# Performance work log

Measured on AMD Instinct MI355X. Metric: run time of the kernel, lower is better.

The kernel has to match this reference:

```python
import math
import jax, jax.numpy as jnp
import numpy as np

B, D, T, C, H = 4096, 1024, 768, 16, 4
CURV = 0.05
EPS = 1e-8
ASINH_MAX = float(np.arcsinh(2.0 ** 15))

# ---------- Poincare ball ops (hyptorch.pmath) ----------

def artanh(x):
    x = jnp.clip(x, -1 + 1e-5, 1 - 1e-5)
    return 0.5 * (jnp.log1p(x) - jnp.log1p(-x))

def p_logmap0(y, c):
    sc = c ** 0.5
    n = jnp.clip(jnp.linalg.norm(y, axis=-1, keepdims=True), 1e-15, None)
    return y / (n * sc) * artanh(sc * n)

def p_expmap0(u, c):
    sc = c ** 0.5
    n = jnp.clip(jnp.linalg.norm(u, axis=-1, keepdims=True), 1e-15, None)
    return jnp.tanh(sc * n) * u / (sc * n)

def p_project(x, c):
    maxn = (1 - 4e-3) / c ** 0.5  # float32 eps in hyptorch
    n = jnp.clip(jnp.linalg.norm(x, axis=-1, keepdims=True), 1e-15, None)
    return jnp.where(n > maxn, x / n * maxn, x)

# ---------- Lorentz ops (MERU-style L module) ----------

def l_expmap0(x, c):
    rc = (c ** 0.5) * jnp.linalg.norm(x, axis=-1, keepdims=True)
    si = jnp.clip(rc, EPS, ASINH_MAX)
    return jnp.sinh(si) * x / jnp.clip(rc, EPS, None)

def l_logmap0(x, c):
    rc = (c ** 0.5) * jnp.linalg.norm(x, axis=-1, keepdims=True)
    return jnp.arcsinh(rc) * x / jnp.clip(rc, EPS, None)

def oxy_angle(x, y, c):
    xt = jnp.sqrt(1.0 / c + jnp.sum(x * x, -1))
    yt = jnp.sqrt(1.0 / c + jnp.sum(y * y, -1))
    c_xyl = c * (jnp.sum(x * y, -1) - xt * yt)
    num = yt + c_xyl * xt
    den = jnp.sqrt(jnp.clip(c_xyl ** 2 - 1.0, EPS, None))
    acos_in = num / (jnp.linalg.norm(x, axis=-1) * den + EPS)
    return jnp.arccos(jnp.clip(acos_in, -1 + EPS, 1 - EPS))

def half_aperture(x, c, min_radius=0.1):
    asin_in = 2.0 * min_radius / (jnp.linalg.norm(x, axis=-1) * c ** 0.5 + EPS)
    return jnp.arcsin(jnp.clip(asin_in, -1 + EPS, 1 - EPS))

# ---------- small building blocks ----------

def layernorm(x, w, b, eps=1e-5):
    mu = jnp.mean(x, -1, keepdims=True)
    var = jnp.mean((x - mu) ** 2, -1, keepdims=True)
    return (x - mu) * jax.lax.rsqrt(var + eps) * w + b

def mha(x, w_in, b_in, w_out, b_out):
    # x: (B, S=4, D), torch nn.MultiheadAttention, batch_first, 4 heads
    Bq, S, Dm = x.shape
    hd = Dm // H
    qkv = x @ w_in.T + b_in
    q, k, v = jnp.split(qkv, 3, axis=-1)
    rs = lambda t: t.reshape(Bq, S, H, hd).transpose(0, 2, 1, 3)
    q, k, v = rs(q), rs(k), rs(v)
    a = jax.nn.softmax(jnp.einsum('bhqd,bhkd->bhqk', q, k) / math.sqrt(hd), axis=-1)
    o = jnp.einsum('bhqk,bhkd->bhqd', a, v).transpose(0, 2, 1, 3).reshape(Bq, S, Dm)
    return o @ w_out.T + b_out

def mobius_add_batch(x, y, c):
    # x: (C, D) (the -p points), y: (B, D) -> (C, B, D)
    xy = x @ y.T                               # (C, B)
    x2 = jnp.sum(x * x, -1, keepdims=True)     # (C, 1)
    y2 = jnp.sum(y * y, -1)                    # (B,)
    num = (1 + 2 * c * xy + c * y2[None, :])[..., None] * x[:, None, :] \
        + (1 - c * x2)[..., None] * y[None, :, :]
    den = 1 + 2 * c * xy + c * c * x2 * y2[None, :]
    return num / (den[..., None] + 1e-5)

def hyperbolic_mlr(x, a, p, c):
    sc = c ** 0.5
    p_p = p_expmap0(p, c)                      # (C, D)
    conf = 1 - c * jnp.sum(p_p ** 2, -1, keepdims=True)
    a_p = a * conf                             # (C, D)
    lam = 2.0 / (1 - c * jnp.sum(p_p ** 2, -1))
    a_norm = jnp.linalg.norm(a_p, axis=-1)     # (C,)
    kk = lam * a_norm / sc
    mob = mobius_add_batch(-p_p, x, c)         # (C, B, D)
    num = 2 * sc * jnp.einsum('cbd,cd->cb', mob, a_p)
    den = a_norm[:, None] * (1 - c * jnp.sum(mob ** 2, -1))
    return (kk[:, None] * jnp.arcsinh(num / den)).T  # (B, C)

def hyp_loss_fn(order_hyp, family_hyp, order, family, mask,
                to_w, to_b, tf_w, tf_b):
    order_feats = l_expmap0(order @ to_w.T + to_b, CURV)
    order_loss = jnp.mean(jax.nn.relu(
        oxy_angle(order_feats, family_hyp, CURV) - half_aperture(order_feats, CURV)))
    fam_feats = l_expmap0(family @ tf_w.T + tf_b, CURV)
    fpen = jax.nn.relu(
        oxy_angle(fam_feats, order_hyp, CURV) - half_aperture(fam_feats, CURV))
    m = mask.astype(order.dtype)
    cnt = jnp.sum(m)
    family_loss = jnp.where(cnt > 0, jnp.sum(fpen * m) / jnp.clip(cnt, 1.0, None), 0.0)
    return order_loss + family_loss


def setup_inputs() -> dict:
    key = jax.random.key(0)
    ks = jax.random.split(key, 20)
    g = lambda k, s, sc: jax.random.normal(k, s, jnp.float32) * sc
    inp = {
        # Poincare-ball points: scale down so sqrt(c)*||x|| << 1
        'order_hyp': g(ks[0], (B, D), 0.02),
        'family_hyp': g(ks[1], (B, D), 0.02),
        'order_euc': g(ks[2], (B, D), 1.0),
        'family_euc': g(ks[3], (B, D), 1.0),
        'order': g(ks[4], (B, T), 1.0),
        'family': g(ks[5], (B, T), 1.0),
        'mask': jax.random.randint(ks[6], (B,), 0, 2, jnp.int32),
        # MultiheadAttention params
        'in_proj_w': g(ks[7], (3 * D, D), D ** -0.5),
        'in_proj_b': jnp.zeros((3 * D,), jnp.float32),
        'out_proj_w': g(ks[8], (D, D), D ** -0.5),
        'out_proj_b': jnp.zeros((D,), jnp.float32),
        # LayerNorm
        'ln_w': jnp.ones((D,), jnp.float32),
        'ln_b': jnp.zeros((D,), jnp.float32),
        # text projections
        'to_w': g(ks[9], (D, T), T ** -0.5),
        'to_b': jnp.zeros((D,), jnp.float32),
        'tf_w': g(ks[10], (D, T), T ** -0.5),
        'tf_b': jnp.zeros((D,), jnp.float32),
        # HyperbolicMLR params
        'mlr_a': g(ks[11], (C, D), 0.02),
        'mlr_p': g(ks[12], (C, D), 0.02),
    }
    return inp


def reference(order_hyp, family_hyp, order_euc, family_euc, order, family, mask,
              in_proj_w, in_proj_b, out_proj_w, out_proj_b, ln_w, ln_b,
              to_w, to_b, tf_w, tf_b, mlr_a, mlr_p):
    # FromPoincare (logmap0 on the ball)
    fh_e = p_logmap0(family_hyp, CURV)
    oh_e = p_logmap0(order_hyp, CURV)
    gf = jnp.stack([oh_e, fh_e, order_euc, family_euc], axis=1)  # (B, 4, D)
    attn = mha(gf, in_proj_w, in_proj_b, out_proj_w, out_proj_b)
    gf = layernorm(gf + attn, ln_w, ln_b)
    oh, fh, oeu, feu = gf[:, 0], gf[:, 1], gf[:, 2], gf[:, 3]
    fh = l_expmap0(fh, CURV)
    oh = l_expmap0(oh, CURV)
    hyp_loss = hyp_loss_fn(oh, fh, order, family, mask, to_w, to_b, tf_w, tf_b)
    oh_out = l_logmap0(oh, CURV)
    hyp_pt = p_project(p_expmap0(oh_out, CURV), CURV)  # ToPoincare(riemannian=False)
    logits = hyperbolic_mlr(hyp_pt, mlr_a, mlr_p, CURV)
    return (logits, hyp_loss, oh, fh, oeu, feu)
```

## Files before the change

kernel.cpp:

```cpp
#include <hip/hip_runtime.h>
#include <stdint.h>

#define BB    4096
#define DD    1024
#define TT    768
#define CC    16
#define HH    4
#define SS    4
#define HD    256
#define M1    (BB*SS)
#define CURVF 0.05f
#define SCF   0.22360679774997896f
#define EPSF  1e-8f
#define ASINH_MAXF 11.090354888959125f

#define OFF_LOGITS 0ull
#define OFF_LOSS   65536ull
#define OFF_OH     65537ull
#define OFF_FH     (65537ull + 4194304ull)
#define OFF_OEU    (65537ull + 2ull*4194304ull)
#define OFF_FEU    (65537ull + 3ull*4194304ull)

typedef __attribute__((ext_vector_type(8))) short bf16x8;
typedef __attribute__((ext_vector_type(4))) float f32x4;

__device__ __forceinline__ float bf2f(unsigned short h) {
  union { unsigned int u; float f; } v; v.u = ((unsigned int)h) << 16; return v.f;
}
__device__ __forceinline__ unsigned short f2bf(float f) {
  union { float f; unsigned int u; } v; v.f = f;
  unsigned int u = v.u;
  return (unsigned short)((u + 0x7FFFu + ((u >> 16) & 1u)) >> 16);
}
__device__ __forceinline__ ushort4 f2bf4(float4 v) {
  ushort4 o; o.x = f2bf(v.x); o.y = f2bf(v.y); o.z = f2bf(v.z); o.w = f2bf(v.w);
  return o;
}
__device__ __forceinline__ float wsum(float v) {
#pragma unroll
  for (int o = 32; o > 0; o >>= 1) v += __shfl_xor(v, o, 64);
  return v;
}
__device__ __forceinline__ float block_sum(float v, float* red) {
  v = wsum(v);
  int lane = threadIdx.x & 63, wv = threadIdx.x >> 6;
  __syncthreads();
  if (lane == 0) red[wv] = v;
  __syncthreads();
  return red[0] + red[1] + red[2] + red[3];
}
__device__ __forceinline__ float artanh_clip(float x) {
  x = fminf(fmaxf(x, -1.0f + 1e-5f), 1.0f - 1e-5f);
  return 0.5f * (log1pf(x) - log1pf(-x));
}

typedef __attribute__((address_space(1))) const void gas_void;
typedef __attribute__((address_space(3))) void las_void;
__device__ __forceinline__ void gld16(void* l, const void* g) {
  __builtin_amdgcn_global_load_lds((gas_void*)g, (las_void*)l, 16, 0, 0);
}

#define VMCNT(n) asm volatile("s_waitcnt vmcnt(" #n ")" ::: "memory")

struct Cvt6 {
  const float4* src[6];
  unsigned short* dst[6];
  unsigned int end4[6];
};

__device__ __forceinline__ void prep_gf_body(const float* __restrict__ ohyp,
    const float* __restrict__ fhyp, const float* __restrict__ oeuc,
    const float* __restrict__ feuc, unsigned short* __restrict__ gf,
    int b, float* red) {
  int t = threadIdx.x;
  size_t base4 = (size_t)b * (DD / 4);
  float4 xo = ((const float4*)ohyp)[base4 + t];
  float4 xf = ((const float4*)fhyp)[base4 + t];
  float so = xo.x * xo.x + xo.y * xo.y + xo.z * xo.z + xo.w * xo.w;
  float sf = xf.x * xf.x + xf.y * xf.y + xf.z * xf.z + xf.w * xf.w;
  float no2 = block_sum(so, red);
  float nf2 = block_sum(sf, red);
  float no = fmaxf(sqrtf(no2), 1e-15f);
  float nf = fmaxf(sqrtf(nf2), 1e-15f);
  float fo = artanh_clip(SCF * no) / (no * SCF);
  float ff = artanh_clip(SCF * nf) / (nf * SCF);
  size_t g0 = (size_t)b * 4 * (DD / 4);
  float4 e2 = ((const float4*)oeuc)[base4 + t];
  float4 e3 = ((const float4*)feuc)[base4 + t];
  float4 y0 = {xo.x * fo, xo.y * fo, xo.z * fo, xo.w * fo};
  float4 y1 = {xf.x * ff, xf.y * ff, xf.z * ff, xf.w * ff};
  ((ushort4*)gf)[g0 + t]              = f2bf4(y0);
  ((ushort4*)gf)[g0 + DD / 4 + t]     = f2bf4(y1);
  ((ushort4*)gf)[g0 + 2 * DD / 4 + t] = f2bf4(e2);
  ((ushort4*)gf)[g0 + 3 * DD / 4 + t] = f2bf4(e3);
}

__device__ __forceinline__ void mlr_prep_body(const float* __restrict__ a,
    const float* __restrict__ p, float* __restrict__ p_p, float* __restrict__ a_p,
    float* __restrict__ cs, int c, float* red) {
  int t = threadIdx.x;
  size_t base4 = (size_t)c * (DD / 4);
  float4 pv = ((const float4*)p)[base4 + t];
  float4 av = ((const float4*)a)[base4 + t];
  float sp = pv.x * pv.x + pv.y * pv.y + pv.z * pv.z + pv.w * pv.w;
  float sa = av.x * av.x + av.y * av.y + av.z * av.z + av.w * av.w;
  float spa = pv.x * av.x + pv.y * av.y + pv.z * av.z + pv.w * av.w;
  sp = block_sum(sp, red); sa = block_sum(sa, red); spa = block_sum(spa, red);
  float n = fmaxf(sqrtf(sp), 1e-15f);
  float f = tanhf(SCF * n) / (SCF * n);
  float x2 = f * f * sp;
  float conf = 1.0f - CURVF * x2;
  float a_norm = fabsf(conf) * sqrtf(sa);
  float lam = 2.0f / (1.0f - CURVF * x2);
  float kk = lam * a_norm / SCF;
  float xa = -f * conf * spa;
  float4 pp = {pv.x * f, pv.y * f, pv.z * f, pv.w * f};
  float4 ap = {av.x * conf, av.y * conf, av.z * conf, av.w * conf};
  ((float4*)p_p)[base4 + t] = pp;
  ((float4*)a_p)[base4 + t] = ap;
  if (threadIdx.x == 0) {
    cs[c * 5 + 0] = x2; cs[c * 5 + 1] = conf; cs[c * 5 + 2] = a_norm;
    cs[c * 5 + 3] = kk; cs[c * 5 + 4] = xa;
  }
}

__global__ __launch_bounds__(256) void k_front(
    const float* __restrict__ ohyp, const float* __restrict__ fhyp,
    const float* __restrict__ oeuc, const float* __restrict__ feuc,
    unsigned short* __restrict__ gf,
    const float* __restrict__ mlr_a, const float* __restrict__ mlr_p,
    float* __restrict__ p_p, float* __restrict__ a_p, float* __restrict__ cs,
    Cvt6 cv, unsigned int total4) {
  __shared__ float red[4];
  unsigned int blk = blockIdx.x;
  if (blk < BB) {
    prep_gf_body(ohyp, fhyp, oeuc, feuc, gf, (int)blk, red);
    return;
  }
  if (blk < BB + CC) {
    mlr_prep_body(mlr_a, mlr_p, p_p, a_p, cs, (int)(blk - BB), red);
    return;
  }
  unsigned int i = (blk - BB - CC) * 256 + threadIdx.x;
  if (i >= total4) return;
#pragma unroll
  for (int j = 0; j < 6; j++) {
    if (i < cv.end4[j]) {
      unsigned int k = i - (j ? cv.end4[j - 1] : 0u);
      ((ushort4*)cv.dst[j])[k] = f2bf4(cv.src[j][k]);
      return;
    }
  }
}

__device__ __forceinline__ void gemm256_body(
    const unsigned short* __restrict__ A, const unsigned short* __restrict__ Bm,
    const float* __restrict__ bias, void* __restrict__ Cv,
    int N, int K, int bx, int by, int out_bf16,
    unsigned short (*lds)[2][8192]) {
  const long tileM = (long)by * 256;
  const long tileN = (long)bx * 256;
  const int tid = threadIdx.x;
  const int lane = tid & 63;
  const int wv = tid >> 6;
  const int wr = wv >> 2;
  const int wc = wv & 3;
  const int NT = K >> 5;

  f32x4 acc[8][4];
#pragma unroll
  for (int i = 0; i < 8; i++)
#pragma unroll
    for (int j = 0; j < 4; j++) acc[i][j] = (f32x4){0.f, 0.f, 0.f, 0.f};

  const int srow = tid >> 2;
  const int lc = (tid & 3) ^ ((srow >> 1) & 3);
  const unsigned short* Ag = A + (tileM + srow) * (long)K + lc * 8;
  const unsigned short* Bg = Bm + (tileN + srow) * (long)K + lc * 8;

  auto stageA = [&](int t) {
    int b = t & 3;
    const unsigned short* s = Ag + t * 32;
    gld16(&lds[b][0][tid * 8], s);
    gld16(&lds[b][0][4096 + tid * 8], s + (long)128 * K);
  };
  auto stageB = [&](int t) {
    int b = t & 3;
    const unsigned short* s = Bg + t * 32;
    gld16(&lds[b][1][tid * 8], s);
    gld16(&lds[b][1][4096 + tid * 8], s + (long)128 * K);
  };

  stageA(0); stageB(0);
  stageA(1); stageB(1);
  stageA(2); stageB(2);
  VMCNT(8);
  __builtin_amdgcn_s_barrier();
  asm volatile("" ::: "memory");

  const int fr = lane & 15;
  const int hi = lane >> 4;
  const int fko = (hi ^ ((fr >> 1) & 3)) * 8;

  for (int t = 0; t < NT; ++t) {
    const unsigned short* Ab = &lds[t & 3][0][0];
    const unsigned short* Bb = &lds[t & 3][1][0];
    bf16x8 af[4], bfr[4];
#pragma unroll
    for (int j = 0; j < 4; j++)
      bfr[j] = *(const bf16x8*)(Bb + (wc * 64 + j * 16 + fr) * 32 + fko);
#pragma unroll
    for (int i = 0; i < 4; i++)
      af[i] = *(const bf16x8*)(Ab + (wr * 128 + i * 16 + fr) * 32 + fko);
    if (t + 3 < NT) stageA(t + 3);
    __builtin_amdgcn_s_setprio(1);
#pragma unroll
    for (int i = 0; i < 4; i++)
#pragma unroll
      for (int j = 0; j < 4; j++)
        acc[i][j] = __builtin_amdgcn_mfma_f32_16x16x32_bf16(af[i], bfr[j], acc[i][j], 0, 0, 0);
    __builtin_amdgcn_s_setprio(0);
#pragma unroll
    for (int i = 0; i < 4; i++)
      af[i] = *(const bf16x8*)(Ab + (wr * 128 + (i + 4) * 16 + fr) * 32 + fko);
    if (t + 3 < NT) stageB(t + 3);
    __builtin_amdgcn_s_setprio(1);
#pragma unroll
    for (int i = 0; i < 4; i++)
#pragma unroll
      for (int j = 0; j < 4; j++)
        acc[i + 4][j] = __builtin_amdgcn_mfma_f32_16x16x32_bf16(af[i], bfr[j], acc[i + 4][j], 0, 0, 0);
    __builtin_amdgcn_s_setprio(0);
    if (t + 1 < NT) {
      if (t + 3 < NT)      VMCNT(8);
      else if (t + 2 < NT) VMCNT(4);
      else                 VMCNT(0);
      __builtin_amdgcn_s_barrier();
      asm volatile("" ::: "memory");
    }
  }

  const int er = hi * 4;
  if (out_bf16) {
#pragma unroll
    for (int i = 0; i < 8; i++)
#pragma unroll
      for (int j = 0; j < 4; j++) {
        long col = tileN + wc * 64 + j * 16 + fr;
        float bv = bias ? bias[col] : 0.f;
#pragma unroll
        for (int r = 0; r < 4; r++) {
          long row = tileM + wr * 128 + i * 16 + er + r;
          ((unsigned short*)Cv)[row * (long)N + col] = f2bf(acc[i][j][r] + bv);
        }
      }
  } else {
#pragma unroll
    for (int i = 0; i < 8; i++)
#pragma unroll
      for (int j = 0; j < 4; j++) {
        long col = tileN + wc * 64 + j * 16 + fr;
        float bv = bias ? bias[col] : 0.f;
#pragma unroll
        for (int r = 0; r < 4; r++) {
          long row = tileM + wr * 128 + i * 16 + er + r;
          ((float*)Cv)[row * (long)N + col] = acc[i][j][r] + bv;
        }
      }
  }
}

template <int OUT_BF16>
__global__ __launch_bounds__(512) void k_gemm256(
    const unsigned short* __restrict__ A, const unsigned short* __restrict__ Bm,
    const float* __restrict__ bias, void* __restrict__ Cv,
    int N, int K, int nx) {
  __shared__ unsigned short lds[4][2][8192];
  const int nwg = gridDim.x;
  const int rid = blockIdx.x;
  const int wg = (rid & 7) * (nwg >> 3) + (rid >> 3);
  gemm256_body(A, Bm, bias, Cv, N, K, wg % nx, wg / nx, OUT_BF16, lds);
}

__global__ __launch_bounds__(512) void k_gemm_merged(
    const unsigned short* __restrict__ A0, const unsigned short* __restrict__ B0,
    const float* __restrict__ bias0, void* __restrict__ C0, int N0, int K0,
    int nx0, int nwg0,
    const unsigned short* __restrict__ A1, const unsigned short* __restrict__ B1,
    const float* __restrict__ bias1, void* __restrict__ C1,
    const unsigned short* __restrict__ A2, const unsigned short* __restrict__ B2,
    const float* __restrict__ bias2, void* __restrict__ C2,
    int N12, int K12, int nx12, int nwg1) {
  __shared__ unsigned short lds[4][2][8192];
  const int nwg = gridDim.x;
  const int rid = blockIdx.x;
  const int wg = (rid & 7) * (nwg >> 3) + (rid >> 3);
  if (wg < nwg0) {
    gemm256_body(A0, B0, bias0, C0, N0, K0, wg % nx0, wg / nx0, 1, lds);
  } else if (wg < nwg0 + nwg1) {
    int w = wg - nwg0;
    gemm256_body(A1, B1, bias1, C1, N12, K12, w % nx12, w / nx12, 0, lds);
  } else {
    int w = wg - nwg0 - nwg1;
    gemm256_body(A2, B2, bias2, C2, N12, K12, w % nx12, w / nx12, 0, lds);
  }
}

__global__ __launch_bounds__(256) void k_attn(const unsigned short* __restrict__ qkv,
                                              unsigned short* __restrict__ o) {
  int b = blockIdx.x;
  int h = blockIdx.y;
  int lane = threadIdx.x & 63;
  int qi = threadIdx.x >> 6;
  const unsigned short* base = qkv + (size_t)b * 4 * 3072 + h * HD;
  int d = lane * 4;
  float qv[4], kv[4][4], vv[4][4];
  {
    ushort4 q4 = *(const ushort4*)(base + (size_t)qi * 3072 + d);
    qv[0] = bf2f(q4.x); qv[1] = bf2f(q4.y); qv[2] = bf2f(q4.z); qv[3] = bf2f(q4.w);
  }
#pragma unroll
  for (int j = 0; j < 4; j++) {
    ushort4 k4 = *(const ushort4*)(base + (size_t)j * 3072 + 1024 + d);
    ushort4 v4 = *(const ushort4*)(base + (size_t)j * 3072 + 2048 + d);
    kv[j][0] = bf2f(k4.x); kv[j][1] = bf2f(k4.y); kv[j][2] = bf2f(k4.z); kv[j][3] = bf2f(k4.w);
    vv[j][0] = bf2f(v4.x); vv[j][1] = bf2f(v4.y); vv[j][2] = bf2f(v4.z); vv[j][3] = bf2f(v4.w);
  }
  float sc_[4];
#pragma unroll
  for (int j = 0; j < 4; j++) {
    float p = 0.f;
#pragma unroll
    for (int t = 0; t < 4; t++) p += qv[t] * kv[j][t];
    sc_[j] = wsum(p) * (1.0f / 16.0f);
  }
  float mx = fmaxf(fmaxf(sc_[0], sc_[1]), fmaxf(sc_[2], sc_[3]));
  float e[4], den = 0.f;
#pragma unroll
  for (int j = 0; j < 4; j++) { e[j] = expf(sc_[j] - mx); den += e[j]; }
  float inv = 1.0f / den;
  float4 ov = {0.f, 0.f, 0.f, 0.f};
#pragma unroll
  for (int j = 0; j < 4; j++) {
    float w = e[j] * inv;
    ov.x += w * vv[j][0]; ov.y += w * vv[j][1];
    ov.z += w * vv[j][2]; ov.w += w * vv[j][3];
  }
  *(ushort4*)(o + (size_t)(b * 4 + qi) * DD + h * HD + d) = f2bf4(ov);
}

__global__ __launch_bounds__(256) void k_ln_oxy(const unsigned short* __restrict__ gf,
    const unsigned short* __restrict__ attn, const float* __restrict__ lnw,
    const float* __restrict__ lnb, const float* __restrict__ ofeat,
    const float* __restrict__ ffeat, float* __restrict__ pens,
    float* __restrict__ dout) {
  __shared__ float red[4];
  int r = blockIdx.x;
  int b = r >> 2, s = r & 3;
  int t = threadIdx.x;
  size_t base4 = (size_t)r * (DD / 4);
  ushort4 g4 = ((const ushort4*)gf)[base4 + t];
  ushort4 a4 = ((const ushort4*)attn)[base4 + t];
  float x[4] = {bf2f(g4.x) + bf2f(a4.x), bf2f(g4.y) + bf2f(a4.y),
                bf2f(g4.z) + bf2f(a4.z), bf2f(g4.w) + bf2f(a4.w)};
  float sum = x[0] + x[1] + x[2] + x[3];
  float sq = x[0] * x[0] + x[1] * x[1] + x[2] * x[2] + x[3] * x[3];
  sum = block_sum(sum, red);
  sq  = block_sum(sq, red);
  float mu = sum * (1.0f / (float)DD);
  float var = sq * (1.0f / (float)DD) - mu * mu;
  float inv = rsqrtf(var + 1e-5f);
  float4 w4 = ((const float4*)lnw)[t];
  float4 b4 = ((const float4*)lnb)[t];
  float y[4];
  y[0] = (x[0] - mu) * inv * w4.x + b4.x;
  y[1] = (x[1] - mu) * inv * w4.y + b4.y;
  y[2] = (x[2] - mu) * inv * w4.z + b4.z;
  y[3] = (x[3] - mu) * inv * w4.w + b4.w;
  float fmul = 1.0f;
  if (s < 2) {
    float n2 = y[0] * y[0] + y[1] * y[1] + y[2] * y[2] + y[3] * y[3];
    n2 = block_sum(n2, red);
    float rc = SCF * sqrtf(n2);
    float si = fminf(fmaxf(rc, EPSF), ASINH_MAXF);
    fmul = sinhf(si) / fmaxf(rc, EPSF);
  }
  size_t offs = (s == 0) ? OFF_OH : (s == 1) ? OFF_FH : (s == 2) ? OFF_OEU : OFF_FEU;
  float4* outp = (float4*)(dout + offs + (size_t)b * DD);
  float4 o4 = {y[0] * fmul, y[1] * fmul, y[2] * fmul, y[3] * fmul};
  outp[t] = o4;

  if (s < 2) {
    const float* raw = (s == 0) ? ffeat : ofeat;
    float4 rv = ((const float4*)(raw + (size_t)b * DD))[t];
    float sxx = rv.x * rv.x + rv.y * rv.y + rv.z * rv.z + rv.w * rv.w;
    float sxy = rv.x * o4.x + rv.y * o4.y + rv.z * o4.z + rv.w * o4.w;
    float syy = o4.x * o4.x + o4.y * o4.y + o4.z * o4.z + o4.w * o4.w;
    sxx = block_sum(sxx, red);
    sxy = block_sum(sxy, red);
    syy = block_sum(syy, red);
    if (t == 0) {
      float nraw = sqrtf(sxx);
      float rc2 = SCF * nraw;
      float si2 = fminf(fmaxf(rc2, EPSF), ASINH_MAXF);
      float f = sinhf(si2) / fmaxf(rc2, EPSF);
      float x2 = f * f * sxx;
      float xy = f * sxy;
      float y2 = syy;
      float nx = f * nraw;
      float xt = sqrtf(1.0f / CURVF + x2);
      float yt = sqrtf(1.0f / CURVF + y2);
      float c_xyl = CURVF * (xy - xt * yt);
      float num = yt + c_xyl * xt;
      float den = sqrtf(fmaxf(c_xyl * c_xyl - 1.0f, EPSF));
      float ai = num / (nx * den + EPSF);
      ai = fminf(fmaxf(ai, -1.0f + EPSF), 1.0f - EPSF);
      float ang = acosf(ai);
      float asi = 0.2f / (nx * SCF + EPSF);
      asi = fminf(fmaxf(asi, -1.0f + EPSF), 1.0f - EPSF);
      float ap = asinf(asi);
      int which = (s == 0) ? 1 : 0;
      pens[(size_t)which * BB + b] = fmaxf(ang - ap, 0.0f);
    }
  }
}

__global__ __launch_bounds__(256) void k_back(const float* __restrict__ oh,
    const float* __restrict__ p_p, const float* __restrict__ a_p,
    const float* __restrict__ cs, float* __restrict__ logits,
    const float* __restrict__ pens, const int* __restrict__ mask,
    float* __restrict__ dout) {
  __shared__ float row[DD];
  __shared__ float dots[CC][2];
  __shared__ float s_n2;
  __shared__ float red[4];
  int blk = blockIdx.x;
  int lane = threadIdx.x & 63, wv = threadIdx.x >> 6;

  if (blk == BB) {
    float s0 = 0.f, s1 = 0.f, cnt = 0.f;
    for (int i = threadIdx.x; i < BB; i += 256) {
      s0 += pens[i];
      float m = (float)mask[i];
      s1 += pens[BB + i] * m;
      cnt += m;
    }
    s0 = block_sum(s0, red);
    s1 = block_sum(s1, red);
    cnt = block_sum(cnt, red);
    if (threadIdx.x == 0) {
      float order_loss = s0 / (float)BB;
      float fam = (cnt > 0.f) ? s1 / fmaxf(cnt, 1.0f) : 0.0f;
      dout[OFF_LOSS] = order_loss + fam;
    }
    return;
  }

  int b = blk;
  const float* src = oh + (size_t)b * DD;
#pragma unroll
  for (int k = 0; k < 4; k++)
    row[threadIdx.x + 256 * k] = src[threadIdx.x + 256 * k];
  __syncthreads();
  if (wv == 0) {
    float n2p = 0.f;
#pragma unroll
    for (int k = 0; k < 4; k++) {
      float4 v = ((const float4*)row)[lane + 64 * k];
      n2p += v.x * v.x + v.y * v.y + v.z * v.z + v.w * v.w;
    }
    n2p = wsum(n2p);
    if (lane == 0) s_n2 = n2p;
  }
#pragma unroll
  for (int ccc = 0; ccc < 4; ccc++) {
    int c = wv * 4 + ccc;
    const float4* pp4 = (const float4*)(p_p + (size_t)c * DD);
    const float4* ap4 = (const float4*)(a_p + (size_t)c * DD);
    float dp = 0.f, da = 0.f;
#pragma unroll
    for (int k = 0; k < 4; k++) {
      int d4 = lane + 64 * k;
      float4 v = ((const float4*)row)[d4];
      float4 p4 = pp4[d4];
      float4 a4 = ap4[d4];
      dp += p4.x * v.x + p4.y * v.y + p4.z * v.z + p4.w * v.w;
      da += a4.x * v.x + a4.y * v.y + a4.z * v.z + a4.w * v.w;
    }
    dp = wsum(dp); da = wsum(da);
    if (lane == 0) { dots[c][0] = dp; dots[c][1] = da; }
  }
  __syncthreads();
  if (threadIdx.x < CC) {
    int c = threadIdx.x;
    float n2 = s_n2;
    float n1 = sqrtf(n2);
    float rc = SCF * n1;
    float g = asinhf(rc) / fmaxf(rc, EPSF);
    float nu = fmaxf(n1 * g, 1e-15f);
    float fac = tanhf(SCF * nu) / (SCF * nu);
    float s = g * fac;
    float ny = fmaxf(n1 * s, 1e-15f);
    float maxn = (1.0f - 0.004f) / SCF;
    if (ny > maxn) s *= maxn / ny;
    float y2 = s * s * n2;
    float py = s * dots[c][0];
    float ay = s * dots[c][1];
    float x2 = cs[c * 5 + 0], conf = cs[c * 5 + 1], a_norm = cs[c * 5 + 2];
    float kk = cs[c * 5 + 3], xa = cs[c * 5 + 4];
    float xy = -py;
    float A = 1.f + 2.f * CURVF * xy + CURVF * y2;
    float den0 = 1.f + 2.f * CURVF * xy + CURVF * CURVF * x2 * y2;
    float d = den0 + 1e-5f;
    float num = 2.f * SCF * (A * xa + conf * ay) / d;
    float mob2 = (A * A * x2 + 2.f * A * conf * xy + conf * conf * y2) / (d * d);
    float denl = a_norm * (1.f - CURVF * mob2);
    logits[(size_t)b * CC + c] = kk * asinhf(num / denl);
  }
}

extern "C" void kernel_launch(void* const* d_in, const int* in_sizes, int n_in,
                              void* d_out, int out_size, void* d_ws, size_t ws_size,
                              hipStream_t stream) {
  const float* order_hyp  = (const float*)d_in[0];
  const float* family_hyp = (const float*)d_in[1];
  const float* order_euc  = (const float*)d_in[2];
  const float* family_euc = (const float*)d_in[3];
  const float* order      = (const float*)d_in[4];
  const float* family     = (const float*)d_in[5];
  const int*   mask       = (const int*)d_in[6];
  const float* in_proj_w  = (const float*)d_in[7];
  const float* in_proj_b  = (const float*)d_in[8];
  const float* out_proj_w = (const float*)d_in[9];
  const float* out_proj_b = (const float*)d_in[10];
  const float* ln_w       = (const float*)d_in[11];
  const float* ln_b       = (const float*)d_in[12];
  const float* to_w       = (const float*)d_in[13];
  const float* to_b       = (const float*)d_in[14];
  const float* tf_w       = (const float*)d_in[15];
  const float* tf_b       = (const float*)d_in[16];
  const float* mlr_a      = (const float*)d_in[17];
  const float* mlr_p      = (const float*)d_in[18];
  float* dout = (float*)d_out;

  char* w = (char*)d_ws;
  size_t off = 0;
  auto take = [&](size_t n) { char* p = w + off; off += (n + 255) & ~(size_t)255; return p; };
  unsigned short* gf_bf   = (unsigned short*)take((size_t)M1 * DD * 2);
  unsigned short* region2 = (unsigned short*)take((size_t)M1 * 3 * DD * 2);
  unsigned short* o_bf    = (unsigned short*)take((size_t)M1 * DD * 2);
  unsigned short* win_bf  = (unsigned short*)take((size_t)3 * DD * DD * 2);
  unsigned short* wout_bf = (unsigned short*)take((size_t)DD * DD * 2);
  unsigned short* tow_bf  = (unsigned short*)take((size_t)DD * TT * 2);
  unsigned short* tfw_bf  = (unsigned short*)take((size_t)DD * TT * 2);
  unsigned short* ord_bf  = (unsigned short*)take((size_t)BB * TT * 2);
  unsigned short* fam_bf  = (unsigned short*)take((size_t)BB * TT * 2);
  float* p_p   = (float*)take((size_t)CC * DD * 4);
  float* a_p   = (float*)take((size_t)CC * DD * 4);
  float* cs    = (float*)take(CC * 5 * 4);
  float* pens  = (float*)take((size_t)2 * BB * 4);
  float* ofeat = (float*)take((size_t)BB * DD * 4);
  float* ffeat = (float*)take((size_t)BB * DD * 4);

  unsigned short* qkv     = region2;
  unsigned short* attn_bf = region2;

  Cvt6 cv;
  cv.src[0] = (const float4*)in_proj_w;  cv.dst[0] = win_bf;
  cv.src[1] = (const float4*)out_proj_w; cv.dst[1] = wout_bf;
  cv.src[2] = (const float4*)to_w;       cv.dst[2] = tow_bf;
  cv.src[3] = (const float4*)tf_w;       cv.dst[3] = tfw_bf;
  cv.src[4] = (const float4*)order;      cv.dst[4] = ord_bf;
  cv.src[5] = (const float4*)family;     cv.dst[5] = fam_bf;
  unsigned int n4[6] = {3u * DD * DD / 4, DD * DD / 4, DD * TT / 4, DD * TT / 4,
                        BB * TT / 4, BB * TT / 4};
  unsigned int acc4 = 0;
  for (int j = 0; j < 6; j++) { acc4 += n4[j]; cv.end4[j] = acc4; }
  unsigned int cvtBlocks = (acc4 + 255) / 256;
  k_front<<<BB + CC + cvtBlocks, 256, 0, stream>>>(
      order_hyp, family_hyp, order_euc, family_euc, gf_bf,
      mlr_a, mlr_p, p_p, a_p, cs, cv, acc4);

  {
    int nx0 = 3 * DD / 256, ny0 = M1 / 256;
    int nwg0 = nx0 * ny0;
    int nx12 = DD / 256, ny12 = BB / 256;
    int nwg1 = nx12 * ny12;
    int total = nwg0 + 2 * nwg1;
    k_gemm_merged<<<total, 512, 0, stream>>>(
        gf_bf, win_bf, in_proj_b, qkv, 3 * DD, DD, nx0, nwg0,
        ord_bf, tow_bf, to_b, ofeat,
        fam_bf, tfw_bf, tf_b, ffeat,
        DD, TT, nx12, nwg1);
  }

  k_attn<<<dim3(BB, HH), 256, 0, stream>>>(qkv, o_bf);

  {
    int nx = DD / 256, ny = M1 / 256;
    k_gemm256<1><<<nx * ny, 512, 0, stream>>>(
        o_bf, wout_bf, out_proj_b, attn_bf, DD, DD, nx);
  }

  k_ln_oxy<<<M1, 256, 0, stream>>>(gf_bf, attn_bf, ln_w, ln_b,
                                   ofeat, ffeat, pens, dout);

  k_back<<<BB + 1, 256, 0, stream>>>(dout + OFF_OH, p_p, a_p, cs,
                                     dout + OFF_LOGITS, pens, mask, dout);

  (void)in_sizes; (void)n_in; (void)out_size; (void)ws_size;
}
```

Measured before the change: 445.1 us.

## Rework 256x256 GEMM mainloop to K=64 double-buffered, ping-pong scheduled pipeline

```diff
diff --git a/kernel.cpp b/kernel.cpp
--- a/kernel.cpp
+++ b/kernel.cpp
@@ -61,6 +61,7 @@
 }
 
 #define VMCNT(n) asm volatile("s_waitcnt vmcnt(" #n ")" ::: "memory")
+#define BARRIER() do { asm volatile("" ::: "memory"); __builtin_amdgcn_s_barrier(); asm volatile("" ::: "memory"); } while (0)
 
 struct Cvt6 {
   const float4* src[6];
@@ -157,7 +158,7 @@
     const unsigned short* __restrict__ A, const unsigned short* __restrict__ Bm,
     const float* __restrict__ bias, void* __restrict__ Cv,
     int N, int K, int bx, int by, int out_bf16,
-    unsigned short (*lds)[2][8192]) {
+    unsigned short* As, unsigned short* Bs) {
   const long tileM = (long)by * 256;
   const long tileN = (long)bx * 256;
   const int tid = threadIdx.x;
@@ -165,7 +166,7 @@
   const int wv = tid >> 6;
   const int wr = wv >> 2;
   const int wc = wv & 3;
-  const int NT = K >> 5;
+  const int NT = K >> 6;
 
   f32x4 acc[8][4];
 #pragma unroll
@@ -173,72 +174,91 @@
 #pragma unroll
     for (int j = 0; j < 4; j++) acc[i][j] = (f32x4){0.f, 0.f, 0.f, 0.f};
 
-  const int srow = tid >> 2;
-  const int lc = (tid & 3) ^ ((srow >> 1) & 3);
-  const unsigned short* Ag = A + (tileM + srow) * (long)K + lc * 8;
-  const unsigned short* Bg = Bm + (tileN + srow) * (long)K + lc * 8;
-
-  auto stageA = [&](int t) {
-    int b = t & 3;
-    const unsigned short* s = Ag + t * 32;
-    gld16(&lds[b][0][tid * 8], s);
-    gld16(&lds[b][0][4096 + tid * 8], s + (long)128 * K);
-  };
-  auto stageB = [&](int t) {
-    int b = t & 3;
-    const unsigned short* s = Bg + t * 32;
-    gld16(&lds[b][1][tid * 8], s);
-    gld16(&lds[b][1][4096 + tid * 8], s + (long)128 * K);
-  };
-
-  stageA(0); stageB(0);
-  stageA(1); stageB(1);
-  stageA(2); stageB(2);
-  VMCNT(8);
-  __builtin_amdgcn_s_barrier();
-  asm volatile("" ::: "memory");
+  const int srow = tid >> 3;
+  const int sc = (tid & 7) ^ (srow & 7);
+  const unsigned short* Ag = A + (tileM + srow) * (long)K + sc * 8;
+  const unsigned short* Bg = Bm + (tileN + srow) * (long)K + sc * 8;
+
+#define STAGE_A(T_) do { \
+    unsigned short* d_ = As + ((T_) & 1) * 16384; \
+    const unsigned short* g_ = Ag + (long)(T_) * 64; \
+    gld16(d_ + tid * 8,          g_); \
+    gld16(d_ + 4096 + tid * 8,   g_ + (long)64 * K); \
+    gld16(d_ + 8192 + tid * 8,   g_ + (long)128 * K); \
+    gld16(d_ + 12288 + tid * 8,  g_ + (long)192 * K); } while (0)
+#define STAGE_BLO(T_) do { \
+    unsigned short* d_ = Bs + ((T_) & 1) * 16384; \
+    const unsigned short* g_ = Bg + (long)(T_) * 64; \
+    gld16(d_ + tid * 8,          g_); \
+    gld16(d_ + 4096 + tid * 8,   g_ + (long)64 * K); } while (0)
+#define STAGE_BHI(T_) do { \
+    unsigned short* d_ = Bs + ((T_) & 1) * 16384 + 8192; \
+    const unsigned short* g_ = Bg + (long)(T_) * 64 + (long)128 * K; \
+    gld16(d_ + tid * 8,          g_); \
+    gld16(d_ + 4096 + tid * 8,   g_ + (long)64 * K); } while (0)
 
   const int fr = lane & 15;
   const int hi = lane >> 4;
-  const int fko = (hi ^ ((fr >> 1) & 3)) * 8;
-
-  for (int t = 0; t < NT; ++t) {
-    const unsigned short* Ab = &lds[t & 3][0][0];
-    const unsigned short* Bb = &lds[t & 3][1][0];
-    bf16x8 af[4], bfr[4];
-#pragma unroll
-    for (int j = 0; j < 4; j++)
-      bfr[j] = *(const bf16x8*)(Bb + (wc * 64 + j * 16 + fr) * 32 + fko);
-#pragma unroll
-    for (int i = 0; i < 4; i++)
-      af[i] = *(const bf16x8*)(Ab + (wr * 128 + i * 16 + fr) * 32 + fko);
-    if (t + 3 < NT) stageA(t + 3);
-    __builtin_amdgcn_s_setprio(1);
-#pragma unroll
-    for (int i = 0; i < 4; i++)
-#pragma unroll
-      for (int j = 0; j < 4; j++)
-        acc[i][j] = __builtin_amdgcn_mfma_f32_16x16x32_bf16(af[i], bfr[j], acc[i][j], 0, 0, 0);
-    __builtin_amdgcn_s_setprio(0);
-#pragma unroll
-    for (int i = 0; i < 4; i++)
-      af[i] = *(const bf16x8*)(Ab + (wr * 128 + (i + 4) * 16 + fr) * 32 + fko);
-    if (t + 3 < NT) stageB(t + 3);
-    __builtin_amdgcn_s_setprio(1);
-#pragma unroll
-    for (int i = 0; i < 4; i++)
-#pragma unroll
-      for (int j = 0; j < 4; j++)
-        acc[i + 4][j] = __builtin_amdgcn_mfma_f32_16x16x32_bf16(af[i], bfr[j], acc[i + 4][j], 0, 0, 0);
-    __builtin_amdgcn_s_setprio(0);
-    if (t + 1 < NT) {
-      if (t + 3 < NT)      VMCNT(8);
-      else if (t + 2 < NT) VMCNT(4);
-      else                 VMCNT(0);
-      __builtin_amdgcn_s_barrier();
-      asm volatile("" ::: "memory");
-    }
-  }
+  const int fx = fr & 7;
+  const unsigned short* ArdBase = As + wr * 8192 + fr * 64;
+  const unsigned short* BrdBase = Bs + (wc >> 1) * 8192 + (wc & 1) * 4096 + fr * 64;
+
+#define LDA8(dst_, p_, ihsel_) do { \
+    const unsigned short* b_ = ArdBase + (p_) * 16384 + (ihsel_) * 4096; \
+    _Pragma("unroll") for (int i2_ = 0; i2_ < 4; i2_++) \
+    _Pragma("unroll") for (int s_ = 0; s_ < 2; s_++) \
+      dst_[i2_][s_] = *(const bf16x8*)(b_ + i2_ * 1024 + ((s_ * 4 + hi) ^ fx) * 8); } while (0)
+#define LDB4(dst_, p_, jhsel_) do { \
+    const unsigned short* b_ = BrdBase + (p_) * 16384 + (jhsel_) * 2048; \
+    _Pragma("unroll") for (int j2_ = 0; j2_ < 2; j2_++) \
+    _Pragma("unroll") for (int s_ = 0; s_ < 2; s_++) \
+      dst_[j2_][s_] = *(const bf16x8*)(b_ + j2_ * 1024 + ((s_ * 4 + hi) ^ fx) * 8); } while (0)
+#define MFMA16(ihsel_, jhsel_, a_, b_) do { \
+    __builtin_amdgcn_s_setprio(1); \
+    _Pragma("unroll") for (int i2_ = 0; i2_ < 4; i2_++) \
+    _Pragma("unroll") for (int j2_ = 0; j2_ < 2; j2_++) { \
+      acc[(ihsel_)*4 + i2_][(jhsel_)*2 + j2_] = __builtin_amdgcn_mfma_f32_16x16x32_bf16( \
+          a_[i2_][0], b_[j2_][0], acc[(ihsel_)*4 + i2_][(jhsel_)*2 + j2_], 0, 0, 0); \
+      acc[(ihsel_)*4 + i2_][(jhsel_)*2 + j2_] = __builtin_amdgcn_mfma_f32_16x16x32_bf16( \
+          a_[i2_][1], b_[j2_][1], acc[(ihsel_)*4 + i2_][(jhsel_)*2 + j2_], 0, 0, 0); \
+    } \
+    __builtin_amdgcn_s_setprio(0); } while (0)
+
+  STAGE_A(0); STAGE_BLO(0); STAGE_BHI(0); STAGE_A(1);
+  VMCNT(4);
+  BARRIER();
+
+  bf16x8 a_[4][2], b0_[2][2], b1_[2][2];
+  for (int T = 0; T < NT; ++T) {
+    const int p = T & 1;
+    LDA8(a_, p, 0);
+    LDB4(b0_, p, 0);
+    if (T + 1 < NT) STAGE_BLO(T + 1);
+    BARRIER();
+    MFMA16(0, 0, a_, b0_);
+    BARRIER();
+    LDB4(b1_, p, 1);
+    if (T + 1 < NT) STAGE_BHI(T + 1);
+    BARRIER();
+    MFMA16(0, 1, a_, b1_);
+    BARRIER();
+    LDA8(a_, p, 1);
+    BARRIER();
+    MFMA16(1, 1, a_, b1_);
+    BARRIER();
+    if (T + 2 < NT) { STAGE_A(T + 2); VMCNT(4); }
+    else            { VMCNT(0); }
+    BARRIER();
+    MFMA16(1, 0, a_, b0_);
+    BARRIER();
+  }
+
+#undef STAGE_A
+#undef STAGE_BLO
+#undef STAGE_BHI
+#undef LDA8
+#undef LDB4
+#undef MFMA16
 
   const int er = hi * 4;
   if (out_bf16) {
@@ -271,18 +291,19 @@
 }
 
 template <int OUT_BF16>
-__global__ __launch_bounds__(512) void k_gemm256(
+__global__ __launch_bounds__(512, 2) void k_gemm256(
     const unsigned short* __restrict__ A, const unsigned short* __restrict__ Bm,
     const float* __restrict__ bias, void* __restrict__ Cv,
     int N, int K, int nx) {
-  __shared__ unsigned short lds[4][2][8192];
+  __shared__ unsigned short As[2 * 2 * 128 * 64];
+  __shared__ unsigned short Bs[2 * 2 * 128 * 64];
   const int nwg = gridDim.x;
   const int rid = blockIdx.x;
   const int wg = (rid & 7) * (nwg >> 3) + (rid >> 3);
-  gemm256_body(A, Bm, bias, Cv, N, K, wg % nx, wg / nx, OUT_BF16, lds);
-}
-
-__global__ __launch_bounds__(512) void k_gemm_merged(
+  gemm256_body(A, Bm, bias, Cv, N, K, wg % nx, wg / nx, OUT_BF16, As, Bs);
+}
+
+__global__ __launch_bounds__(512, 2) void k_gemm_merged(
     const unsigned short* __restrict__ A0, const unsigned short* __restrict__ B0,
     const float* __restrict__ bias0, void* __restrict__ C0, int N0, int K0,
     int nx0, int nwg0,
@@ -291,18 +312,19 @@
     const unsigned short* __restrict__ A2, const unsigned short* __restrict__ B2,
     const float* __restrict__ bias2, void* __restrict__ C2,
     int N12, int K12, int nx12, int nwg1) {
-  __shared__ unsigned short lds[4][2][8192];
+  __shared__ unsigned short As[2 * 2 * 128 * 64];
+  __shared__ unsigned short Bs[2 * 2 * 128 * 64];
   const int nwg = gridDim.x;
   const int rid = blockIdx.x;
   const int wg = (rid & 7) * (nwg >> 3) + (rid >> 3);
   if (wg < nwg0) {
-    gemm256_body(A0, B0, bias0, C0, N0, K0, wg % nx0, wg / nx0, 1, lds);
+    gemm256_body(A0, B0, bias0, C0, N0, K0, wg % nx0, wg / nx0, 1, As, Bs);
   } else if (wg < nwg0 + nwg1) {
     int w = wg - nwg0;
-    gemm256_body(A1, B1, bias1, C1, N12, K12, w % nx12, w / nx12, 0, lds);
+    gemm256_body(A1, B1, bias1, C1, N12, K12, w % nx12, w / nx12, 0, As, Bs);
   } else {
     int w = wg - nwg0 - nwg1;
-    gemm256_body(A2, B2, bias2, C2, N12, K12, w % nx12, w / nx12, 0, lds);
+    gemm256_body(A2, B2, bias2, C2, N12, K12, w % nx12, w / nx12, 0, As, Bs);
   }
 }
 
```

After: 464.8 us. 1.04x slower.
